# Kernel tuning notes

Measured on AMD Instinct MI355X. Metric: run time of the kernel, lower is better.

Reference implementation:

```python
import jax, jax.numpy as jnp
import numpy as np

HEAD = 16
EMB = 1024
D_K = EMB // HEAD


def setup_inputs() -> dict:
    key = jax.random.key(0)
    ks = jax.random.split(key, 11)
    B, S, E = 2, 2048, EMB
    scale = 1.0 / np.sqrt(E)
    inp = {
        "query": jax.random.normal(ks[0], (B, S, E), jnp.float32),
        "key": jax.random.normal(ks[1], (B, S, E), jnp.float32),
        "value": jax.random.normal(ks[2], (B, S, E), jnp.float32),
        "Wq": jax.random.normal(ks[3], (E, E), jnp.float32) * scale,
        "bq": jnp.zeros((E,), jnp.float32),
        "Wk": jax.random.normal(ks[4], (E, E), jnp.float32) * scale,
        "bk": jnp.zeros((E,), jnp.float32),
        "Wv": jax.random.normal(ks[5], (E, E), jnp.float32) * scale,
        "bv": jnp.zeros((E,), jnp.float32),
        "Wo": jax.random.normal(ks[6], (E, E), jnp.float32) * scale,
        "bo": jnp.zeros((E,), jnp.float32),
    }
    return inp


def reference(query, key, value, Wq, bq, Wk, bk, Wv, bv, Wo, bo):
    B, S, E = query.shape
    # 3 input projections, split into heads: [B, H, S, d_k]
    def proj(x, W, b):
        return (x @ W.T + b).reshape(B, S, HEAD, D_K).transpose(0, 2, 1, 3)

    q = proj(query, Wq, bq)
    k = proj(key, Wk, bk)
    v = proj(value, Wv, bv)

    # scaled dot-product attention (full matrix, as in original)
    scores = jnp.einsum("bhqd,bhkd->bhqk", q, k) / jnp.sqrt(jnp.float32(D_K))
    attn = jax.nn.softmax(scores, axis=-1)  # dropout in eval mode = identity
    x = jnp.einsum("bhqk,bhkd->bhqd", attn, v)

    # merge heads and output projection
    x = x.transpose(0, 2, 1, 3).reshape(B, S, E)
    return x @ Wo.T + bo
```

## Files before the change

kernel.cpp:

```cpp
#include <hip/hip_runtime.h>
#include <hip/hip_bf16.h>
#include <math.h>


constexpr int Sn = 2048;
constexpr int En = 1024;
constexpr int Hn = 16;
constexpr int Dk = 64;
constexpr int Kn = 1024;
constexpr size_t WSZ = 1048576;
constexpr size_t TSZ = 4194304;

#define QSCALE 0.18033688011112042f

typedef __bf16 bf16x8 __attribute__((ext_vector_type(8)));
typedef float  f32x4  __attribute__((ext_vector_type(4)));
typedef float  f32x16 __attribute__((ext_vector_type(16)));

union U16 { uint4 u; bf16x8 v; __hip_bfloat16 h[8]; };
union U8  { uint2 u; __hip_bfloat162 h2[2]; __hip_bfloat16 h[4]; };
union U4  { unsigned u; __hip_bfloat162 h2; };

__device__ inline U16 cvt8f(const float* __restrict__ p) {
    float4 a = *(const float4*)p;
    float4 b = *(const float4*)(p + 4);
    U16 r;
    r.h[0] = __float2bfloat16(a.x); r.h[1] = __float2bfloat16(a.y);
    r.h[2] = __float2bfloat16(a.z); r.h[3] = __float2bfloat16(a.w);
    r.h[4] = __float2bfloat16(b.x); r.h[5] = __float2bfloat16(b.y);
    r.h[6] = __float2bfloat16(b.z); r.h[7] = __float2bfloat16(b.w);
    return r;
}

__device__ inline void gload16(const __hip_bfloat16* g, __hip_bfloat16* l) {
    __builtin_amdgcn_global_load_lds(
        (const __attribute__((address_space(1))) void*)g,
        (__attribute__((address_space(3))) void*)l, 16, 0, 0);
}

template<int ROWS, int NW>
__device__ inline void stage_tile(const __hip_bfloat16* __restrict__ src, int ld,
                                  __hip_bfloat16* lds, int w, int lane) {
    int l8 = lane >> 3;
    int g = (lane & 7) ^ (l8 & 7);
    #pragma unroll
    for (int j = 0; j < ROWS / (8 * NW); ++j) {
        int c = j * NW + w;
        gload16(src + (size_t)(c * 8 + l8) * ld + g * 8, lds + c * 512);
    }
}

__global__ __launch_bounds__(256)
void cvt_all(const float* __restrict__ q, const float* __restrict__ k,
             const float* __restrict__ v,
             const float* __restrict__ w0, const float* __restrict__ w1,
             const float* __restrict__ w2, const float* __restrict__ w3,
             __hip_bfloat16* __restrict__ xdst, __hip_bfloat16* __restrict__ wdst)
{
    int bx = blockIdx.x;
    const float* src;
    __hip_bfloat16* dst;
    size_t base;
    if (bx < 6144) {
        int z = bx >> 11;
        src = (z == 0) ? q : (z == 1) ? k : v;
        dst = xdst + (size_t)z * TSZ;
        base = ((size_t)(bx & 2047) * 256 + threadIdx.x) * 8;
    } else {
        int y = (bx - 6144) >> 9;
        src = (y == 0) ? w0 : (y == 1) ? w1 : (y == 2) ? w2 : w3;
        dst = wdst + (size_t)y * WSZ;
        base = ((size_t)((bx - 6144) & 511) * 256 + threadIdx.x) * 8;
    }
    U16 r = cvt8f(src + base);
    *(uint4*)&dst[base] = r.u;
}

template<int NT>
__device__ inline void gemm_core(const __hip_bfloat16* __restrict__ Ab,
                                 const __hip_bfloat16* __restrict__ Wb,
                                 __hip_bfloat16* As, __hip_bfloat16* Bs,
                                 f32x4 (&acc)[2][NT], int w, int lane)
{
    const int l15 = lane & 15, lg = lane >> 4, l7 = lane & 7;
    const int wm = (w & 1) * 32, wn = (w >> 1) * (NT * 16);
    const int coff0 = (lg ^ l7) * 8;
    const int coff1 = ((4 + lg) ^ l7) * 8;

    #pragma unroll
    for (int i = 0; i < 2; ++i)
        #pragma unroll
        for (int j = 0; j < NT; ++j) acc[i][j] = {0.f, 0.f, 0.f, 0.f};

    for (int k0 = 0; k0 < Kn; k0 += 64) {
        stage_tile<64, 4>(Ab + k0, Kn, As, w, lane);
        stage_tile<NT * 32, 4>(Wb + k0, Kn, Bs, w, lane);
        __syncthreads();

        U16 af[2][2], bf[NT][2];
        #pragma unroll
        for (int mt = 0; mt < 2; ++mt) {
            int r = (wm + mt * 16 + l15) * 64;
            af[mt][0].u = *(const uint4*)&As[r + coff0];
            af[mt][1].u = *(const uint4*)&As[r + coff1];
        }
        #pragma unroll
        for (int nt = 0; nt < NT; ++nt) {
            int r = (wn + nt * 16 + l15) * 64;
            bf[nt][0].u = *(const uint4*)&Bs[r + coff0];
            bf[nt][1].u = *(const uint4*)&Bs[r + coff1];
        }
        #pragma unroll
        for (int mt = 0; mt < 2; ++mt)
            #pragma unroll
            for (int nt = 0; nt < NT; ++nt) {
                acc[mt][nt] = __builtin_amdgcn_mfma_f32_16x16x32_bf16(af[mt][0].v, bf[nt][0].v, acc[mt][nt], 0, 0, 0);
                acc[mt][nt] = __builtin_amdgcn_mfma_f32_16x16x32_bf16(af[mt][1].v, bf[nt][1].v, acc[mt][nt], 0, 0, 0);
            }
        __syncthreads();
    }
}

__global__ __launch_bounds__(256)
void gemm_qkv(const __hip_bfloat16* __restrict__ X, const __hip_bfloat16* __restrict__ Wall,
              const float* __restrict__ bq, const float* __restrict__ bk,
              const float* __restrict__ bv, __hip_bfloat16* __restrict__ outbase)
{
    __shared__ __align__(16) __hip_bfloat16 As[64 * 64];
    __shared__ __align__(16) __hip_bfloat16 Bs[128 * 64];

    const int tid = threadIdx.x, w = tid >> 6, lane = tid & 63;
    const int z = blockIdx.z;
    const int blockM = blockIdx.x * 64, blockN = blockIdx.y * 128;

    f32x4 acc[2][4];
    gemm_core<4>(X + (size_t)z * TSZ + (size_t)blockM * Kn,
                 Wall + (size_t)z * WSZ + (size_t)blockN * Kn,
                 As, Bs, acc, w, lane);

    const float scale = (z == 0) ? QSCALE : 1.0f;
    const float* bias = (z == 0) ? bq : (z == 1) ? bk : bv;
    __hip_bfloat16* out = outbase + (size_t)z * TSZ;

    const int l15 = lane & 15, lg = lane >> 4;
    const int wm = (w & 1) * 32, wn = (w >> 1) * 64;

    #pragma unroll
    for (int nt = 0; nt < 4; ++nt) {
        int n = blockN + wn + nt * 16 + l15;
        float bvn = bias[n] * scale;
        int h_ = n >> 6, d_ = n & 63;
        #pragma unroll
        for (int mt = 0; mt < 2; ++mt) {
            int m0 = blockM + wm + mt * 16 + lg * 4;
            int b_ = m0 >> 11, s_ = m0 & (Sn - 1);
            if (z < 2) {
                #pragma unroll
                for (int i = 0; i < 4; ++i)
                    out[(((size_t)b_ * Hn + h_) * Sn + s_ + i) * Dk + d_] =
                        __float2bfloat16(fmaf(acc[mt][nt][i], scale, bvn));
            } else {
                U8 pk;
                #pragma unroll
                for (int i = 0; i < 4; ++i)
                    pk.h[i] = __float2bfloat16(fmaf(acc[mt][nt][i], scale, bvn));
                *(uint2*)&out[(((size_t)b_ * Hn + h_) * Dk + d_) * Sn + s_] = pk.u;
            }
        }
    }
}

__global__ __launch_bounds__(256)
void gemm_out(const __hip_bfloat16* __restrict__ A, const __hip_bfloat16* __restrict__ W,
              const float* __restrict__ bias, float* __restrict__ out)
{
    __shared__ __align__(16) __hip_bfloat16 As[64 * 64];
    __shared__ __align__(16) __hip_bfloat16 Bs[64 * 64];

    const int tid = threadIdx.x, w = tid >> 6, lane = tid & 63;
    const int blockM = blockIdx.x * 64, blockN = blockIdx.y * 64;

    f32x4 acc[2][2];
    gemm_core<2>(A + (size_t)blockM * Kn, W + (size_t)blockN * Kn,
                 As, Bs, acc, w, lane);

    const int l15 = lane & 15, lg = lane >> 4;
    const int wm = (w & 1) * 32, wn = (w >> 1) * 32;

    #pragma unroll
    for (int nt = 0; nt < 2; ++nt) {
        int n = blockN + wn + nt * 16 + l15;
        float bvn = bias[n];
        #pragma unroll
        for (int mt = 0; mt < 2; ++mt) {
            int m0 = blockM + wm + mt * 16 + lg * 4;
            #pragma unroll
            for (int i = 0; i < 4; ++i)
                out[(size_t)(m0 + i) * Kn + n] = acc[mt][nt][i] + bvn;
        }
    }
}

__global__ __launch_bounds__(256)
void attn(const __hip_bfloat16* __restrict__ Q, const __hip_bfloat16* __restrict__ K,
          const __hip_bfloat16* __restrict__ Vt, __hip_bfloat16* __restrict__ X)
{
    __shared__ __align__(16) __hip_bfloat16 Ks[2][64 * 64];
    __shared__ __align__(16) __hip_bfloat16 Vts[2][64 * 64];
    __shared__ float Lc[2][64];

    const int bh = blockIdx.x, q0 = blockIdx.y * 64;
    const int tid = threadIdx.x, w = tid >> 6, lane = tid & 63;
    const int qs = w >> 1, kh = w & 1;
    const int l31 = lane & 31, hi = lane >> 5;

    const __hip_bfloat16* Qb = Q  + (size_t)bh * Sn * Dk;
    const __hip_bfloat16* Kb = K  + (size_t)bh * Sn * Dk;
    const __hip_bfloat16* Vb = Vt + (size_t)bh * Dk * Sn;

    U16 qf[4];
    {
        const __hip_bfloat16* qp = Qb + (size_t)(q0 + qs * 32 + l31) * Dk + hi * 8;
        #pragma unroll
        for (int d0t = 0; d0t < 4; ++d0t)
            qf[d0t].u = *(const uint4*)(qp + d0t * 16);
    }

    f32x16 o[2];
    #pragma unroll
    for (int dt = 0; dt < 2; ++dt)
        #pragma unroll
        for (int r = 0; r < 16; ++r) o[dt][r] = 0.f;
    float lpart = 0.f;

    const int rK = kh * 32 + l31;

    stage_tile<64, 4>(Kb, Dk, Ks[0], w, lane);
    stage_tile<64, 4>(Vb, Sn, Vts[0], w, lane);

    auto body = [&](int cur, int tn) {
        __syncthreads();
        if (tn < Sn / 64) {
            stage_tile<64, 4>(Kb + (size_t)tn * 64 * Dk, Dk, Ks[cur ^ 1], w, lane);
            stage_tile<64, 4>(Vb + tn * 64, Sn, Vts[cur ^ 1], w, lane);
        }

        f32x16 st;
        #pragma unroll
        for (int r = 0; r < 16; ++r) st[r] = 0.f;
        #pragma unroll
        for (int d0t = 0; d0t < 4; ++d0t) {
            int col = ((d0t * 2 + hi) ^ (rK & 7)) * 8;
            U16 kf; kf.u = *(const uint4*)&Ks[cur][rK * 64 + col];
            st = __builtin_amdgcn_mfma_f32_32x32x16_bf16(kf.v, qf[d0t].v, st, 0, 0, 0);
        }

        float pv[16];
        #pragma unroll
        for (int r = 0; r < 16; ++r) pv[r] = __builtin_amdgcn_exp2f(st[r]);
        float s01 = (pv[0] + pv[1]) + (pv[2] + pv[3]);
        float s23 = (pv[4] + pv[5]) + (pv[6] + pv[7]);
        float s45 = (pv[8] + pv[9]) + (pv[10] + pv[11]);
        float s67 = (pv[12] + pv[13]) + (pv[14] + pv[15]);
        lpart += (s01 + s23) + (s45 + s67);

        uint wv[8];
        #pragma unroll
        for (int m2 = 0; m2 < 8; ++m2) {
            U4 pk; pk.h2 = __float22bfloat162_rn({pv[2 * m2], pv[2 * m2 + 1]});
            wv[m2] = pk.u;
        }
        asm volatile("v_permlane32_swap_b32 %0, %1" : "+v"(wv[0]), "+v"(wv[2]));
        asm volatile("v_permlane32_swap_b32 %0, %1" : "+v"(wv[1]), "+v"(wv[3]));
        asm volatile("v_permlane32_swap_b32 %0, %1" : "+v"(wv[4]), "+v"(wv[6]));
        asm volatile("v_permlane32_swap_b32 %0, %1" : "+v"(wv[5]), "+v"(wv[7]));
        uint4 pa0 = make_uint4(wv[0], wv[1], wv[2], wv[3]);
        uint4 pa1 = make_uint4(wv[4], wv[5], wv[6], wv[7]);

        #pragma unroll
        for (int j = 0; j < 2; ++j) {
            U16 pau; pau.u = (j == 0) ? pa0 : pa1;
            int k0t = kh * 2 + j;
            #pragma unroll
            for (int dt = 0; dt < 2; ++dt) {
                int rV = dt * 32 + l31;
                int col = ((k0t * 2 + hi) ^ (rV & 7)) * 8;
                U16 vf; vf.u = *(const uint4*)&Vts[cur][rV * 64 + col];
                o[dt] = __builtin_amdgcn_mfma_f32_32x32x16_bf16(pau.v, vf.v, o[dt], 0, 0, 0);
            }
        }
    };

    for (int t = 0; t < Sn / 64; t += 2) {
        body(0, t + 1);
        body(1, t + 2);
    }

    __syncthreads();
    float* Ocomb = (float*)Ks;
    if (kh == 0) {
        #pragma unroll
        for (int dt = 0; dt < 2; ++dt)
            #pragma unroll
            for (int r = 0; r < 16; ++r) {
                int qr = (r & 3) + 8 * (r >> 2) + 4 * hi;
                Ocomb[(qs * 32 + qr) * 64 + dt * 32 + l31] = o[dt][r];
            }
        Lc[qs][lane] = lpart;
    }
    __syncthreads();
    if (kh == 1) {
        #pragma unroll
        for (int dt = 0; dt < 2; ++dt)
            #pragma unroll
            for (int r = 0; r < 16; ++r) {
                int qr = (r & 3) + 8 * (r >> 2) + 4 * hi;
                o[dt][r] += Ocomb[(qs * 32 + qr) * 64 + dt * 32 + l31];
            }
        lpart += Lc[qs][lane];
        lpart += __shfl_xor(lpart, 32, 64);
        float linv = 1.f / lpart;

        float li[16];
        #pragma unroll
        for (int r = 0; r < 16; ++r) {
            int qr = (r & 3) + 8 * (r >> 2) + 4 * hi;
            li[r] = __shfl(linv, qr, 64);
        }

        int b_ = bh >> 4, h_ = bh & (Hn - 1);
        #pragma unroll
        for (int r = 0; r < 16; ++r) {
            int qr = (r & 3) + 8 * (r >> 2) + 4 * hi;
            int sr = q0 + qs * 32 + qr;
            __hip_bfloat16* xp = X + ((size_t)(b_ * Sn + sr)) * En + h_ * Dk + l31;
            xp[0]  = __float2bfloat16(o[0][r] * li[r]);
            xp[32] = __float2bfloat16(o[1][r] * li[r]);
        }
    }
}

extern "C" void kernel_launch(void* const* d_in, const int* in_sizes, int n_in,
                              void* d_out, int out_size, void* d_ws, size_t ws_size,
                              hipStream_t stream)
{
    const float* query = (const float*)d_in[0];
    const float* key   = (const float*)d_in[1];
    const float* value = (const float*)d_in[2];
    const float* Wq = (const float*)d_in[3];
    const float* bq = (const float*)d_in[4];
    const float* Wk = (const float*)d_in[5];
    const float* bk = (const float*)d_in[6];
    const float* Wv = (const float*)d_in[7];
    const float* bv = (const float*)d_in[8];
    const float* Wo = (const float*)d_in[9];
    const float* bo = (const float*)d_in[10];
    float* out = (float*)d_out;

    __hip_bfloat16* xqkv = (__hip_bfloat16*)d_ws;
    __hip_bfloat16* Wbf  = xqkv + 3 * TSZ;
    __hip_bfloat16* QKVw = Wbf + 4 * WSZ;
    __hip_bfloat16* Xw   = xqkv;

    cvt_all<<<8192, 256, 0, stream>>>(query, key, value, Wq, Wk, Wv, Wo, xqkv, Wbf);
    gemm_qkv<<<dim3(64, 8, 3), 256, 0, stream>>>(xqkv, Wbf, bq, bk, bv, QKVw);
    attn<<<dim3(32, Sn / 64), 256, 0, stream>>>(QKVw, QKVw + TSZ, QKVw + 2 * TSZ, Xw);
    gemm_out<<<dim3(64, 16), 256, 0, stream>>>(Xw, Wbf + 3 * WSZ, bo, out);
}
```

Measured before the change: 227.8 us.

## Double-buffer QKV GEMM shared tiles and enlarge block tile to 128x128

The QKV projection GEMM now uses a 128x128 output tile per block instead of 64x128, with each wave computing a 64x64 sub-tile (4x4 MFMA fragments). Shared memory tiles are double-buffered, so the next K-slice is staged while MFMAs run on the current one, and there is one barrier per iteration. This aims to raise operand reuse and hide global load latency. In exchange it uses more registers and LDS (64KB) and launches half as many blocks (768), which can reduce occupancy.

Measured after the change: 229.3 us. Within noise of the previous version (+0.7%).

```diff
diff --git a/kernel.cpp b/kernel.cpp
--- a/kernel.cpp
+++ b/kernel.cpp
@@ -126,24 +126,63 @@
               const float* __restrict__ bq, const float* __restrict__ bk,
               const float* __restrict__ bv, __hip_bfloat16* __restrict__ outbase)
 {
-    __shared__ __align__(16) __hip_bfloat16 As[64 * 64];
-    __shared__ __align__(16) __hip_bfloat16 Bs[128 * 64];
+    __shared__ __align__(16) __hip_bfloat16 As[2][128 * 64];
+    __shared__ __align__(16) __hip_bfloat16 Bs[2][128 * 64];
 
     const int tid = threadIdx.x, w = tid >> 6, lane = tid & 63;
     const int z = blockIdx.z;
-    const int blockM = blockIdx.x * 64, blockN = blockIdx.y * 128;
-
-    f32x4 acc[2][4];
-    gemm_core<4>(X + (size_t)z * TSZ + (size_t)blockM * Kn,
-                 Wall + (size_t)z * WSZ + (size_t)blockN * Kn,
-                 As, Bs, acc, w, lane);
+    const int blockM = blockIdx.x * 128, blockN = blockIdx.y * 128;
+    const int l15 = lane & 15, lg = lane >> 4, l7 = lane & 7;
+    const int wm = (w & 1) * 64, wn = (w >> 1) * 64;
+    const int coff0 = (lg ^ l7) * 8;
+    const int coff1 = ((4 + lg) ^ l7) * 8;
+
+    const __hip_bfloat16* Ab = X + (size_t)z * TSZ + (size_t)blockM * Kn;
+    const __hip_bfloat16* Wb = Wall + (size_t)z * WSZ + (size_t)blockN * Kn;
+
+    f32x4 acc[4][4];
+    #pragma unroll
+    for (int i = 0; i < 4; ++i)
+        #pragma unroll
+        for (int j = 0; j < 4; ++j) acc[i][j] = {0.f, 0.f, 0.f, 0.f};
+
+    stage_tile<128, 4>(Ab, Kn, As[0], w, lane);
+    stage_tile<128, 4>(Wb, Kn, Bs[0], w, lane);
+    __syncthreads();
+
+    for (int k0 = 0; k0 < Kn; k0 += 64) {
+        const int cur = (k0 >> 6) & 1;
+        if (k0 + 64 < Kn) {
+            stage_tile<128, 4>(Ab + k0 + 64, Kn, As[cur ^ 1], w, lane);
+            stage_tile<128, 4>(Wb + k0 + 64, Kn, Bs[cur ^ 1], w, lane);
+        }
+
+        U16 af[4][2], bf[4][2];
+        #pragma unroll
+        for (int mt = 0; mt < 4; ++mt) {
+            int r = (wm + mt * 16 + l15) * 64;
+            af[mt][0].u = *(const uint4*)&As[cur][r + coff0];
+            af[mt][1].u = *(const uint4*)&As[cur][r + coff1];
+        }
+        #pragma unroll
+        for (int nt = 0; nt < 4; ++nt) {
+            int r = (wn + nt * 16 + l15) * 64;
+            bf[nt][0].u = *(const uint4*)&Bs[cur][r + coff0];
+            bf[nt][1].u = *(const uint4*)&Bs[cur][r + coff1];
+        }
+        #pragma unroll
+        for (int mt = 0; mt < 4; ++mt)
+            #pragma unroll
+            for (int nt = 0; nt < 4; ++nt) {
+                acc[mt][nt] = __builtin_amdgcn_mfma_f32_16x16x32_bf16(af[mt][0].v, bf[nt][0].v, acc[mt][nt], 0, 0, 0);
+                acc[mt][nt] = __builtin_amdgcn_mfma_f32_16x16x32_bf16(af[mt][1].v, bf[nt][1].v, acc[mt][nt], 0, 0, 0);
+            }
+        __syncthreads();
+    }
 
     const float scale = (z == 0) ? QSCALE : 1.0f;
     const float* bias = (z == 0) ? bq : (z == 1) ? bk : bv;
     __hip_bfloat16* out = outbase + (size_t)z * TSZ;
-
-    const int l15 = lane & 15, lg = lane >> 4;
-    const int wm = (w & 1) * 32, wn = (w >> 1) * 64;
 
     #pragma unroll
     for (int nt = 0; nt < 4; ++nt) {
@@ -151,7 +190,7 @@
         float bvn = bias[n] * scale;
         int h_ = n >> 6, d_ = n & 63;
         #pragma unroll
-        for (int mt = 0; mt < 2; ++mt) {
+        for (int mt = 0; mt < 4; ++mt) {
             int m0 = blockM + wm + mt * 16 + lg * 4;
             int b_ = m0 >> 11, s_ = m0 & (Sn - 1);
             if (z < 2) {
@@ -363,7 +402,7 @@
     __hip_bfloat16* Xw   = xqkv;
 
     cvt_all<<<8192, 256, 0, stream>>>(query, key, value, Wq, Wk, Wv, Wo, xqkv, Wbf);
-    gemm_qkv<<<dim3(64, 8, 3), 256, 0, stream>>>(xqkv, Wbf, bq, bk, bv, QKVw);
+    gemm_qkv<<<dim3(32, 8, 3), 256, 0, stream>>>(xqkv, Wbf, bq, bk, bv, QKVw);
     attn<<<dim3(32, Sn / 64), 256, 0, stream>>>(QKVw, QKVw + TSZ, QKVw + 2 * TSZ, Xw);
     gemm_out<<<dim3(64, 16), 256, 0, stream>>>(Xw, Wbf + 3 * WSZ, bo, out);
 }
```

## Fuse fp32-to-bf16 activation conversion into QKV GEMM A-tile staging

Applied to the files above, without the earlier changes.

The QKV projection GEMM now reads fp32 activations directly, converts them to bf16 in registers, and writes them into swizzled LDS, instead of relying on a separate pass that converts all activations to bf16 in global memory. The conversion kernel now handles only the weights, so the round trip of about 48 MB through global memory for the activations goes away. In exchange, each A tile is reloaded as fp32 once per N-block (8 times), and the synchronous register staging replaces the async global_load_lds path for A. The shared gemm_core helper is inlined into both GEMM kernels, and the workspace layout is adjusted so the attention output gets its own buffer.

New measurement: 238.9 us. +4.9%, slower.

```diff
diff --git a/kernel.cpp b/kernel.cpp
--- a/kernel.cpp
+++ b/kernel.cpp
@@ -50,54 +50,63 @@
     }
 }
 
+__device__ inline void stage_A_f32(const float* __restrict__ src, int ld,
+                                   __hip_bfloat16* As, int tid) {
+    int r = tid >> 2;
+    int p0 = (tid & 3) * 2;
+    const float* sp = src + (size_t)r * ld + p0 * 8;
+    U16 a = cvt8f(sp);
+    U16 b = cvt8f(sp + 8);
+    int sw = r & 7;
+    *(uint4*)&As[r * 64 + ((p0 ^ sw) * 8)]       = a.u;
+    *(uint4*)&As[r * 64 + (((p0 + 1) ^ sw) * 8)] = b.u;
+}
+
 __global__ __launch_bounds__(256)
-void cvt_all(const float* __restrict__ q, const float* __restrict__ k,
-             const float* __restrict__ v,
-             const float* __restrict__ w0, const float* __restrict__ w1,
-             const float* __restrict__ w2, const float* __restrict__ w3,
-             __hip_bfloat16* __restrict__ xdst, __hip_bfloat16* __restrict__ wdst)
-{
-    int bx = blockIdx.x;
-    const float* src;
-    __hip_bfloat16* dst;
-    size_t base;
-    if (bx < 6144) {
-        int z = bx >> 11;
-        src = (z == 0) ? q : (z == 1) ? k : v;
-        dst = xdst + (size_t)z * TSZ;
-        base = ((size_t)(bx & 2047) * 256 + threadIdx.x) * 8;
-    } else {
-        int y = (bx - 6144) >> 9;
-        src = (y == 0) ? w0 : (y == 1) ? w1 : (y == 2) ? w2 : w3;
-        dst = wdst + (size_t)y * WSZ;
-        base = ((size_t)((bx - 6144) & 511) * 256 + threadIdx.x) * 8;
-    }
-    U16 r = cvt8f(src + base);
-    *(uint4*)&dst[base] = r.u;
-}
-
-template<int NT>
-__device__ inline void gemm_core(const __hip_bfloat16* __restrict__ Ab,
-                                 const __hip_bfloat16* __restrict__ Wb,
-                                 __hip_bfloat16* As, __hip_bfloat16* Bs,
-                                 f32x4 (&acc)[2][NT], int w, int lane)
-{
+void cvt_w(const float* __restrict__ w0, const float* __restrict__ w1,
+           const float* __restrict__ w2, const float* __restrict__ w3,
+           __hip_bfloat16* __restrict__ dst)
+{
+    int y = blockIdx.y;
+    const float* src = (y == 0) ? w0 : (y == 1) ? w1 : (y == 2) ? w2 : w3;
+    size_t i = ((size_t)blockIdx.x * 256 + threadIdx.x) * 8;
+    U16 r = cvt8f(src + i);
+    *(uint4*)&dst[(size_t)y * WSZ + i] = r.u;
+}
+
+__global__ __launch_bounds__(256)
+void gemm_qkv(const float* __restrict__ Xq, const float* __restrict__ Xk,
+              const float* __restrict__ Xv, const __hip_bfloat16* __restrict__ Wall,
+              const float* __restrict__ bq, const float* __restrict__ bk,
+              const float* __restrict__ bv, __hip_bfloat16* __restrict__ outbase)
+{
+    __shared__ __align__(16) __hip_bfloat16 As[64 * 64];
+    __shared__ __align__(16) __hip_bfloat16 Bs[128 * 64];
+
+    const int tid = threadIdx.x, w = tid >> 6, lane = tid & 63;
+    const int z = blockIdx.z;
+    const int blockM = blockIdx.x * 64, blockN = blockIdx.y * 128;
     const int l15 = lane & 15, lg = lane >> 4, l7 = lane & 7;
-    const int wm = (w & 1) * 32, wn = (w >> 1) * (NT * 16);
+    const int wm = (w & 1) * 32, wn = (w >> 1) * 64;
     const int coff0 = (lg ^ l7) * 8;
     const int coff1 = ((4 + lg) ^ l7) * 8;
 
+    const float* Xz = (z == 0) ? Xq : (z == 1) ? Xk : Xv;
+    const float* Ab = Xz + (size_t)blockM * Kn;
+    const __hip_bfloat16* Wb = Wall + (size_t)z * WSZ + (size_t)blockN * Kn;
+
+    f32x4 acc[2][4];
     #pragma unroll
     for (int i = 0; i < 2; ++i)
         #pragma unroll
-        for (int j = 0; j < NT; ++j) acc[i][j] = {0.f, 0.f, 0.f, 0.f};
+        for (int j = 0; j < 4; ++j) acc[i][j] = {0.f, 0.f, 0.f, 0.f};
 
     for (int k0 = 0; k0 < Kn; k0 += 64) {
-        stage_tile<64, 4>(Ab + k0, Kn, As, w, lane);
-        stage_tile<NT * 32, 4>(Wb + k0, Kn, Bs, w, lane);
-        __syncthreads();
-
-        U16 af[2][2], bf[NT][2];
+        stage_A_f32(Ab + k0, Kn, As, tid);
+        stage_tile<128, 4>(Wb + k0, Kn, Bs, w, lane);
+        __syncthreads();
+
+        U16 af[2][2], bf[4][2];
         #pragma unroll
         for (int mt = 0; mt < 2; ++mt) {
             int r = (wm + mt * 16 + l15) * 64;
@@ -105,7 +114,7 @@
             af[mt][1].u = *(const uint4*)&As[r + coff1];
         }
         #pragma unroll
-        for (int nt = 0; nt < NT; ++nt) {
+        for (int nt = 0; nt < 4; ++nt) {
             int r = (wn + nt * 16 + l15) * 64;
             bf[nt][0].u = *(const uint4*)&Bs[r + coff0];
             bf[nt][1].u = *(const uint4*)&Bs[r + coff1];
@@ -113,37 +122,16 @@
         #pragma unroll
         for (int mt = 0; mt < 2; ++mt)
             #pragma unroll
-            for (int nt = 0; nt < NT; ++nt) {
+            for (int nt = 0; nt < 4; ++nt) {
                 acc[mt][nt] = __builtin_amdgcn_mfma_f32_16x16x32_bf16(af[mt][0].v, bf[nt][0].v, acc[mt][nt], 0, 0, 0);
                 acc[mt][nt] = __builtin_amdgcn_mfma_f32_16x16x32_bf16(af[mt][1].v, bf[nt][1].v, acc[mt][nt], 0, 0, 0);
             }
         __syncthreads();
     }
-}
-
-__global__ __launch_bounds__(256)
-void gemm_qkv(const __hip_bfloat16* __restrict__ X, const __hip_bfloat16* __restrict__ Wall,
-              const float* __restrict__ bq, const float* __restrict__ bk,
-              const float* __restrict__ bv, __hip_bfloat16* __restrict__ outbase)
-{
-    __shared__ __align__(16) __hip_bfloat16 As[64 * 64];
-    __shared__ __align__(16) __hip_bfloat16 Bs[128 * 64];
-
-    const int tid = threadIdx.x, w = tid >> 6, lane = tid & 63;
-    const int z = blockIdx.z;
-    const int blockM = blockIdx.x * 64, blockN = blockIdx.y * 128;
-
-    f32x4 acc[2][4];
-    gemm_core<4>(X + (size_t)z * TSZ + (size_t)blockM * Kn,
-                 Wall + (size_t)z * WSZ + (size_t)blockN * Kn,
-                 As, Bs, acc, w, lane);
 
     const float scale = (z == 0) ? QSCALE : 1.0f;
     const float* bias = (z == 0) ? bq : (z == 1) ? bk : bv;
     __hip_bfloat16* out = outbase + (size_t)z * TSZ;
-
-    const int l15 = lane & 15, lg = lane >> 4;
-    const int wm = (w & 1) * 32, wn = (w >> 1) * 64;
 
     #pragma unroll
     for (int nt = 0; nt < 4; ++nt) {
@@ -179,13 +167,47 @@
 
     const int tid = threadIdx.x, w = tid >> 6, lane = tid & 63;
     const int blockM = blockIdx.x * 64, blockN = blockIdx.y * 64;
+    const int l15 = lane & 15, lg = lane >> 4, l7 = lane & 7;
+    const int wm = (w & 1) * 32, wn = (w >> 1) * 32;
+    const int coff0 = (lg ^ l7) * 8;
+    const int coff1 = ((4 + lg) ^ l7) * 8;
 
     f32x4 acc[2][2];
-    gemm_core<2>(A + (size_t)blockM * Kn, W + (size_t)blockN * Kn,
-                 As, Bs, acc, w, lane);
-
-    const int l15 = lane & 15, lg = lane >> 4;
-    const int wm = (w & 1) * 32, wn = (w >> 1) * 32;
+    #pragma unroll
+    for (int i = 0; i < 2; ++i)
+        #pragma unroll
+        for (int j = 0; j < 2; ++j) acc[i][j] = {0.f, 0.f, 0.f, 0.f};
+
+    const __hip_bfloat16* Ab = A + (size_t)blockM * Kn;
+    const __hip_bfloat16* Wb = W + (size_t)blockN * Kn;
+
+    for (int k0 = 0; k0 < Kn; k0 += 64) {
+        stage_tile<64, 4>(Ab + k0, Kn, As, w, lane);
+        stage_tile<64, 4>(Wb + k0, Kn, Bs, w, lane);
+        __syncthreads();
+
+        U16 af[2][2], bf[2][2];
+        #pragma unroll
+        for (int mt = 0; mt < 2; ++mt) {
+            int r = (wm + mt * 16 + l15) * 64;
+            af[mt][0].u = *(const uint4*)&As[r + coff0];
+            af[mt][1].u = *(const uint4*)&As[r + coff1];
+        }
+        #pragma unroll
+        for (int nt = 0; nt < 2; ++nt) {
+            int r = (wn + nt * 16 + l15) * 64;
+            bf[nt][0].u = *(const uint4*)&Bs[r + coff0];
+            bf[nt][1].u = *(const uint4*)&Bs[r + coff1];
+        }
+        #pragma unroll
+        for (int mt = 0; mt < 2; ++mt)
+            #pragma unroll
+            for (int nt = 0; nt < 2; ++nt) {
+                acc[mt][nt] = __builtin_amdgcn_mfma_f32_16x16x32_bf16(af[mt][0].v, bf[nt][0].v, acc[mt][nt], 0, 0, 0);
+                acc[mt][nt] = __builtin_amdgcn_mfma_f32_16x16x32_bf16(af[mt][1].v, bf[nt][1].v, acc[mt][nt], 0, 0, 0);
+            }
+        __syncthreads();
+    }
 
     #pragma unroll
     for (int nt = 0; nt < 2; ++nt) {
@@ -357,13 +379,12 @@
     const float* bo = (const float*)d_in[10];
     float* out = (float*)d_out;
 
-    __hip_bfloat16* xqkv = (__hip_bfloat16*)d_ws;
-    __hip_bfloat16* Wbf  = xqkv + 3 * TSZ;
+    __hip_bfloat16* Wbf  = (__hip_bfloat16*)d_ws;
     __hip_bfloat16* QKVw = Wbf + 4 * WSZ;
-    __hip_bfloat16* Xw   = xqkv;
-
-    cvt_all<<<8192, 256, 0, stream>>>(query, key, value, Wq, Wk, Wv, Wo, xqkv, Wbf);
-    gemm_qkv<<<dim3(64, 8, 3), 256, 0, stream>>>(xqkv, Wbf, bq, bk, bv, QKVw);
+    __hip_bfloat16* Xw   = QKVw + 3 * TSZ;
+
+    cvt_w<<<dim3(512, 4), 256, 0, stream>>>(Wq, Wk, Wv, Wo, Wbf);
+    gemm_qkv<<<dim3(64, 8, 3), 256, 0, stream>>>(query, key, value, Wbf, bq, bk, bv, QKVw);
     attn<<<dim3(32, Sn / 64), 256, 0, stream>>>(QKVw, QKVw + TSZ, QKVw + 2 * TSZ, Xw);
     gemm_out<<<dim3(64, 16), 256, 0, stream>>>(Xw, Wbf + 3 * WSZ, bo, out);
 }
```
